# Performance work log

Hardware: AMD Instinct MI355X
Metric: run time of the kernel (lower is better)

The kernel has to match this reference:

```python
import jax, jax.numpy as jnp
import numpy as np

B, S, D = 4, 2048, 1024
H, DQ, DV = 16, 64, 64
LN_EPS = 1e-3  # keras LayerNormalization default


def _layer_norm(x, gamma, beta):
    mu = jnp.mean(x, axis=-1, keepdims=True)
    var = jnp.mean(jnp.square(x - mu), axis=-1, keepdims=True)
    return (x - mu) * jax.lax.rsqrt(var + LN_EPS) * gamma + beta


def setup_inputs() -> dict:
    key = jax.random.key(0)
    ks = jax.random.split(key, 6)
    x = jax.random.normal(ks[0], (B, S, D), jnp.float32)
    lengths = jax.random.randint(ks[1], (B,), 1, S + 1).astype(jnp.int32)
    scale = 0.02
    return {
        "query_sequences": x,
        "key_value_sequences": x,  # identical -> self-attention branch
        "key_value_sequence_lengths": lengths,
        "W_q": jax.random.normal(ks[2], (D, H * DQ), jnp.float32) * scale,
        "b_q": jnp.zeros((H * DQ,), jnp.float32),
        "W_kv": jax.random.normal(ks[3], (D, H * (DQ + DV)), jnp.float32) * scale,
        "b_kv": jnp.zeros((H * (DQ + DV),), jnp.float32),
        "W_o": jax.random.normal(ks[4], (H * DV, D), jnp.float32) * scale,
        "b_o": jnp.zeros((D,), jnp.float32),
        "ln_gamma": jnp.ones((D,), jnp.float32),
        "ln_beta": jnp.zeros((D,), jnp.float32),
    }


def reference(query_sequences, key_value_sequences, key_value_sequence_lengths,
              W_q, b_q, W_kv, b_kv, W_o, b_o, ln_gamma, ln_beta):
    # data-dependent self-attention detection, as in the TF code
    self_att = jnp.all(query_sequences == key_value_sequences)

    q_norm = _layer_norm(query_sequences, ln_gamma, ln_beta)
    kv_used = jnp.where(self_att, _layer_norm(key_value_sequences, ln_gamma, ln_beta),
                        key_value_sequences)
    residual = q_norm

    Q = (q_norm @ W_q + b_q).reshape(B, S, H, DQ)          # b q h d
    KV = kv_used @ W_kv + b_kv
    K = KV[..., : H * DQ].reshape(B, S, H, DQ)              # b k h d
    V = KV[..., H * DQ :].reshape(B, S, H, DV)              # b k h d

    scores = jnp.einsum("bqhd,bkhd->bhqk", Q, K) / np.sqrt(DQ).astype(np.float32)

    # key padding mask: key position < true length
    not_pad = (jnp.arange(S, dtype=jnp.int32)[None, None, None, :]
               < key_value_sequence_lengths[:, None, None, None])
    scores = jnp.where(not_pad, scores, -jnp.inf)
    # in_decoder=False -> no causal mask branch

    attn = jax.nn.softmax(scores, axis=-1)                  # dropout is identity at inference
    ctx = jnp.einsum("bhqk,bkhd->bqhd", attn, V).reshape(B, S, H * DV)
    out = ctx @ W_o + b_o + residual
    return out
```

## Files before the change

kernel.cpp:

```cpp
#include <hip/hip_runtime.h>
#include <hip/hip_bf16.h>
#include <cstdint>
#include <cmath>


#define DEV static __device__ __forceinline__

typedef float  f32x4 __attribute__((ext_vector_type(4)));
typedef short  s16x8 __attribute__((ext_vector_type(8)));
typedef short  s16x4 __attribute__((ext_vector_type(4)));
typedef __bf16 bf16x8 __attribute__((ext_vector_type(8)));
typedef unsigned int u32x4 __attribute__((ext_vector_type(4)));

DEV void gload_lds16(const void* g, void* l) {
  __builtin_amdgcn_global_load_lds(
      (const __attribute__((address_space(1))) unsigned int*)g,
      (__attribute__((address_space(3))) unsigned int*)l, 16, 0, 0);
}

DEV bf16x8 ldsv(const void* p) {
  return __builtin_bit_cast(bf16x8, *(const s16x8*)p);
}

DEV f32x4 mfma16(bf16x8 a, bf16x8 b, f32x4 c) {
  return __builtin_amdgcn_mfma_f32_16x16x32_bf16(a, b, c, 0, 0, 0);
}

DEV unsigned short f2b(float f) {
  __hip_bfloat16 h = __float2bfloat16(f);
  return __builtin_bit_cast(unsigned short, h);
}

DEV unsigned int cvt_pk_bf16(float lo, float hi) {
  unsigned int r;
  asm("v_cvt_pk_bf16_f32 %0, %1, %2" : "=v"(r) : "v"(lo), "v"(hi));
  return r;
}

__global__ __launch_bounds__(256) void ln_kernel(
    const float* __restrict__ x, const float* __restrict__ gamma,
    const float* __restrict__ beta, __hip_bfloat16* __restrict__ out)
{
  const int row = blockIdx.x, t = threadIdx.x;
  const float4 v = ((const float4*)(x + (size_t)row * 1024))[t];
  float s = v.x + v.y + v.z + v.w;
  float q = v.x * v.x + v.y * v.y + v.z * v.z + v.w * v.w;
#pragma unroll
  for (int m = 1; m < 64; m <<= 1) { s += __shfl_xor(s, m, 64); q += __shfl_xor(q, m, 64); }
  __shared__ float red[8];
  if ((t & 63) == 0) { red[t >> 6] = s; red[4 + (t >> 6)] = q; }
  __syncthreads();
  s = red[0] + red[1] + red[2] + red[3];
  q = red[4] + red[5] + red[6] + red[7];
  const float mu = s * (1.f / 1024.f);
  const float var = q * (1.f / 1024.f) - mu * mu;
  const float rs = rsqrtf(var + 1e-3f);
  const float4 g = ((const float4*)gamma)[t];
  const float4 bt = ((const float4*)beta)[t];
  s16x4 o;
  o[0] = (short)f2b((v.x - mu) * rs * g.x + bt.x);
  o[1] = (short)f2b((v.y - mu) * rs * g.y + bt.y);
  o[2] = (short)f2b((v.z - mu) * rs * g.z + bt.z);
  o[3] = (short)f2b((v.w - mu) * rs * g.w + bt.w);
  *(s16x4*)((short*)out + (size_t)row * 1024 + t * 4) = o;
}

__global__ __launch_bounds__(256) void wconv(
    const float* __restrict__ W, int N, __hip_bfloat16* __restrict__ Wt)
{
  __shared__ float tile[64][65];
  const int t = threadIdx.x;
  const int k0 = blockIdx.x * 64, n0 = blockIdx.y * 64;
#pragma unroll
  for (int p = 0; p < 4; ++p) {
    int r = p * 16 + (t >> 4), c4 = (t & 15) * 4;
    float4 v = *(const float4*)(W + (size_t)(k0 + r) * N + n0 + c4);
    tile[r][c4] = v.x; tile[r][c4 + 1] = v.y; tile[r][c4 + 2] = v.z; tile[r][c4 + 3] = v.w;
  }
  __syncthreads();
#pragma unroll
  for (int p = 0; p < 4; ++p) {
    int n = p * 16 + (t >> 4), kc = (t & 15) * 4;
    s16x4 o;
    o[0] = (short)f2b(tile[kc][n]);     o[1] = (short)f2b(tile[kc + 1][n]);
    o[2] = (short)f2b(tile[kc + 2][n]); o[3] = (short)f2b(tile[kc + 3][n]);
    *(s16x4*)((short*)Wt + (size_t)(n0 + n) * 1024 + k0 + kc) = o;
  }
}

template<bool RESID>
__global__ __launch_bounds__(256, 2) void gemm_bt(
    const __hip_bfloat16* __restrict__ A, const __hip_bfloat16* __restrict__ Bt,
    const float* __restrict__ bias0, const float* __restrict__ bias1, int split,
    const __hip_bfloat16* __restrict__ resid,
    __hip_bfloat16* __restrict__ outb, float* __restrict__ outf, int Ncols)
{
  __shared__ __align__(16) short sA[128 * 64];
  __shared__ __align__(16) short sB[128 * 64];
  const int t = threadIdx.x, l = t & 63, w = t >> 6;
  const int wr = w >> 1, wc = w & 1, lr = l & 15, lg = l >> 4;
  const int row0 = blockIdx.y * 128, col0 = blockIdx.x * 128;
  f32x4 acc[4][4] = {};

  for (int kt = 0; kt < 1024; kt += 64) {
#pragma unroll
    for (int p = 0; p < 4; ++p) {
      const int L = p * 4096 + t * 16;
      const int r = L >> 7, c = ((L >> 4) & 7) ^ (r & 7);
      gload_lds16((const char*)A + ((size_t)(row0 + r) * 1024 + kt + c * 8) * 2, (char*)sA + L);
    }
#pragma unroll
    for (int p = 0; p < 4; ++p) {
      const int L = p * 4096 + t * 16;
      const int r = L >> 7, c = ((L >> 4) & 7) ^ (r & 7);
      gload_lds16((const char*)Bt + ((size_t)(col0 + r) * 1024 + kt + c * 8) * 2, (char*)sB + L);
    }
    __syncthreads();

    bf16x8 af[4][2], bfr[4][2];
#pragma unroll
    for (int mb = 0; mb < 4; ++mb) {
      const int ar = wr * 64 + mb * 16 + lr;
#pragma unroll
      for (int kk = 0; kk < 2; ++kk)
        af[mb][kk] = ldsv((const char*)sA + ar * 128 + (((kk * 4 + lg) ^ (ar & 7)) * 16));
    }
#pragma unroll
    for (int nb = 0; nb < 4; ++nb) {
      const int br = wc * 64 + nb * 16 + lr;
#pragma unroll
      for (int kk = 0; kk < 2; ++kk)
        bfr[nb][kk] = ldsv((const char*)sB + br * 128 + (((kk * 4 + lg) ^ (br & 7)) * 16));
    }
#pragma unroll
    for (int kk = 0; kk < 2; ++kk)
#pragma unroll
      for (int mb = 0; mb < 4; ++mb)
#pragma unroll
        for (int nb = 0; nb < 4; ++nb)
          acc[mb][nb] = mfma16(af[mb][kk], bfr[nb][kk], acc[mb][nb]);
    __syncthreads();
  }

#pragma unroll
  for (int mb = 0; mb < 4; ++mb) {
    const int rbase = row0 + wr * 64 + mb * 16 + lg * 4;
#pragma unroll
    for (int nb = 0; nb < 4; ++nb) {
      const int col = col0 + wc * 64 + nb * 16 + lr;
      const float bias = (col < split) ? bias0[col] : bias1[col - split];
#pragma unroll
      for (int jr = 0; jr < 4; ++jr) {
        const size_t idx = (size_t)(rbase + jr) * Ncols + col;
        float v = acc[mb][nb][jr] + bias;
        if (RESID) outf[idx] = v + __bfloat162float(resid[idx]);
        else       outb[idx] = __float2bfloat16(v);
      }
    }
  }
}

__global__ __launch_bounds__(256) void vtrans(
    const __hip_bfloat16* __restrict__ qkv, __hip_bfloat16* __restrict__ vt)
{
  __shared__ __align__(16) short tile[64][72];
  const int t = threadIdx.x;
  const int s0 = blockIdx.x * 64;
  const int bh = blockIdx.y, b = bh >> 4, h = bh & 15;
#pragma unroll
  for (int p = 0; p < 2; ++p) {
    int idx = p * 256 + t;
    int r = idx >> 3, c = idx & 7;
    s16x8 vv = *(const s16x8*)((const short*)qkv +
        (size_t)(b * 2048 + s0 + r) * 3072 + 2048 + h * 64 + c * 8);
    *(s16x8*)((char*)tile + r * 144 + c * 16) = vv;
  }
  __syncthreads();
  const int dv = t >> 2, sc = (t & 3) * 16;
  s16x8 a, bvec;
#pragma unroll
  for (int e = 0; e < 8; ++e) a[e] = tile[sc + e][dv];
#pragma unroll
  for (int e = 0; e < 8; ++e) bvec[e] = tile[sc + 8 + e][dv];
  short* dst = (short*)vt + (size_t)(bh * 64 + dv) * 2048 + s0 + sc;
  *(s16x8*)dst = a;
  *(s16x8*)(dst + 8) = bvec;
}

__global__ __launch_bounds__(256, 4) void attn_kernel(
    const __hip_bfloat16* __restrict__ qkv, const __hip_bfloat16* __restrict__ vt,
    const int* __restrict__ lens, __hip_bfloat16* __restrict__ ctx)
{
  __shared__ __align__(16) short sK[2][64 * 64];
  __shared__ __align__(16) short sV[2][64 * 64];
  const int t = threadIdx.x, l = t & 63, w = t >> 6;
  const int lr = l & 15, lg = l >> 4;
  const int bh = blockIdx.y, b = bh >> 4, h = bh & 15;
  const int q0 = blockIdx.x * 128 + w * 32;
  const int len = lens[b];
  const float NEG = -__builtin_inff();
  const float QSC = 0.18033688f;

  bf16x8 qf[2][2];
#pragma unroll
  for (int mbt = 0; mbt < 2; ++mbt)
#pragma unroll
    for (int kk = 0; kk < 2; ++kk) {
      bf16x8 r = ldsv((const char*)qkv +
          ((size_t)(b * 2048 + q0 + mbt * 16 + lr) * 3072 + h * 64 + kk * 32 + lg * 8) * 2);
#pragma unroll
      for (int e = 0; e < 8; ++e) qf[mbt][kk][e] = (__bf16)((float)r[e] * QSC);
    }

  f32x4 o[4][2] = {};
  float mrun[2] = {NEG, NEG}, ssum[2] = {0.f, 0.f};

  auto stage = [&](short* dK, short* dV, int kv0) {
#pragma unroll
    for (int p = 0; p < 2; ++p) {
      const int L = p * 4096 + t * 16;
      const int r = L >> 7, c = ((L >> 4) & 7) ^ (r & 7);
      gload_lds16((const char*)qkv +
          ((size_t)(b * 2048 + kv0 + r) * 3072 + 1024 + h * 64 + c * 8) * 2, (char*)dK + L);
    }
#pragma unroll
    for (int p = 0; p < 2; ++p) {
      const int L = p * 4096 + t * 16;
      const int r = L >> 7, c = ((L >> 4) & 7) ^ (r & 7);
      gload_lds16((const char*)vt +
          ((size_t)(bh * 64 + r) * 2048 + kv0 + c * 8) * 2, (char*)dV + L);
    }
  };

  const int nt = (len + 63) >> 6;
  short* curK = sK[0]; short* nxtK = sK[1];
  short* curV = sV[0]; short* nxtV = sV[1];
  stage(curK, curV, 0);

  const int srcA = (lg & 1) * 32 + lr;
  const int srcB = srcA + 16;

  for (int ti = 0; ti < nt; ++ti) {
    const int kv0 = ti * 64;
    if (ti + 1 < nt) {
      stage(nxtK, nxtV, kv0 + 64);
      asm volatile("s_waitcnt vmcnt(4)" ::: "memory");
    } else {
      asm volatile("s_waitcnt vmcnt(0)" ::: "memory");
    }
    __builtin_amdgcn_s_barrier();
    asm volatile("" ::: "memory");

    f32x4 sf[2][4] = {};
    __builtin_amdgcn_s_setprio(1);
#pragma unroll
    for (int kk = 0; kk < 2; ++kk) {
      bf16x8 ak[4];
#pragma unroll
      for (int nbt = 0; nbt < 4; ++nbt) {
        const int br = nbt * 16 + lr;
        ak[nbt] = ldsv((const char*)curK + br * 128 + (((kk * 4 + lg) ^ (br & 7)) * 16));
      }
#pragma unroll
      for (int mbt = 0; mbt < 2; ++mbt)
#pragma unroll
        for (int nbt = 0; nbt < 4; ++nbt)
          sf[mbt][nbt] = mfma16(ak[nbt], qf[mbt][kk], sf[mbt][nbt]);
    }
    __builtin_amdgcn_s_setprio(0);

    if (kv0 + 64 > len) {
#pragma unroll
      for (int nbt = 0; nbt < 4; ++nbt)
#pragma unroll
        for (int jr = 0; jr < 4; ++jr)
          if (kv0 + nbt * 16 + lg * 4 + jr >= len) {
            sf[0][nbt][jr] = NEG;
            sf[1][nbt][jr] = NEG;
          }
    }

    float rm[2];
#pragma unroll
    for (int mbt = 0; mbt < 2; ++mbt) {
      f32x4 m4 = sf[mbt][0];
      m4 = __builtin_elementwise_max(m4, sf[mbt][1]);
      m4 = __builtin_elementwise_max(m4, sf[mbt][2]);
      m4 = __builtin_elementwise_max(m4, sf[mbt][3]);
      float m0 = fmaxf(fmaxf(m4[0], m4[1]), fmaxf(m4[2], m4[3]));
      m0 = fmaxf(m0, __shfl_xor(m0, 16, 64));
      m0 = fmaxf(m0, __shfl_xor(m0, 32, 64));
      rm[mbt] = m0;
    }
    const bool need = (rm[0] > mrun[0] + 3.f) || (rm[1] > mrun[1] + 3.f);
    if (__any(need)) {
#pragma unroll
      for (int mbt = 0; mbt < 2; ++mbt) {
        const float mnew = fmaxf(mrun[mbt], rm[mbt]);
        const float corr = __builtin_amdgcn_exp2f(mrun[mbt] - mnew);
        mrun[mbt] = mnew;
        ssum[mbt] *= corr;
#pragma unroll
        for (int nbt2 = 0; nbt2 < 4; ++nbt2) o[nbt2][mbt] *= corr;
      }
    }
    unsigned int W0[2][4], W1[2][4];
#pragma unroll
    for (int mbt = 0; mbt < 2; ++mbt) {
      f32x4 ts = {0.f, 0.f, 0.f, 0.f};
#pragma unroll
      for (int nbt = 0; nbt < 4; ++nbt) {
        f32x4 pe;
#pragma unroll
        for (int jr = 0; jr < 4; ++jr)
          pe[jr] = __builtin_amdgcn_exp2f(sf[mbt][nbt][jr] - mrun[mbt]);
        ts += pe;
        W0[mbt][nbt] = cvt_pk_bf16(pe[0], pe[1]);
        W1[mbt][nbt] = cvt_pk_bf16(pe[2], pe[3]);
      }
      ssum[mbt] += (ts[0] + ts[1]) + (ts[2] + ts[3]);
    }

#pragma unroll
    for (int c = 0; c < 2; ++c) {
      bf16x8 vf[4], pb[2];
#pragma unroll
      for (int nbt2 = 0; nbt2 < 4; ++nbt2) {
        const int vr = nbt2 * 16 + lr;
        vf[nbt2] = ldsv((const char*)curV + vr * 128 + (((c * 4 + lg) ^ (vr & 7)) * 16));
      }
#pragma unroll
      for (int mbt = 0; mbt < 2; ++mbt) {
        const unsigned int selW0 = (lg & 2) ? W0[mbt][2 * c + 1] : W0[mbt][2 * c];
        const unsigned int selW1 = (lg & 2) ? W1[mbt][2 * c + 1] : W1[mbt][2 * c];
        u32x4 bw;
        bw[0] = __shfl((int)selW0, srcA, 64);
        bw[1] = __shfl((int)selW1, srcA, 64);
        bw[2] = __shfl((int)selW0, srcB, 64);
        bw[3] = __shfl((int)selW1, srcB, 64);
        pb[mbt] = __builtin_bit_cast(bf16x8, bw);
      }
      __builtin_amdgcn_s_setprio(1);
#pragma unroll
      for (int nbt2 = 0; nbt2 < 4; ++nbt2)
#pragma unroll
        for (int mbt = 0; mbt < 2; ++mbt)
          o[nbt2][mbt] = mfma16(vf[nbt2], pb[mbt], o[nbt2][mbt]);
      __builtin_amdgcn_s_setprio(0);
    }

    asm volatile("s_waitcnt lgkmcnt(0)" ::: "memory");
    __builtin_amdgcn_s_barrier();
    asm volatile("" ::: "memory");
    short* tk = curK; curK = nxtK; nxtK = tk;
    short* tv = curV; curV = nxtV; nxtV = tv;
  }

  float inv[2];
#pragma unroll
  for (int mbt = 0; mbt < 2; ++mbt) {
    float s = ssum[mbt];
    s += __shfl_xor(s, 16, 64);
    s += __shfl_xor(s, 32, 64);
    inv[mbt] = 1.f / s;
  }
  char* eb = (char*)sK + w * 4352;
#pragma unroll
  for (int mbt = 0; mbt < 2; ++mbt)
#pragma unroll
    for (int nbt2 = 0; nbt2 < 4; ++nbt2)
#pragma unroll
      for (int jr = 0; jr < 4; ++jr)
        *(short*)(eb + (mbt * 16 + lr) * 136 + (nbt2 * 16 + lg * 4 + jr) * 2) =
            (short)f2b(o[nbt2][mbt][jr] * inv[mbt]);
  asm volatile("s_waitcnt lgkmcnt(0)" ::: "memory");
  __builtin_amdgcn_sched_barrier(0);
  const int qi = l >> 1, half = l & 1;
#pragma unroll
  for (int i = 0; i < 4; ++i) {
    s16x8 v = *(const s16x8*)(eb + qi * 136 + half * 64 + i * 16);
    *(s16x8*)((short*)ctx + (size_t)(b * 2048 + q0 + qi) * 1024 + h * 64 + half * 32 + i * 8) = v;
  }
}

extern "C" void kernel_launch(void* const* d_in, const int* in_sizes, int n_in,
                              void* d_out, int out_size, void* d_ws, size_t ws_size,
                              hipStream_t stream)
{
  const float* x     = (const float*)d_in[0];
  const int*   lens  = (const int*)d_in[2];
  const float* Wq    = (const float*)d_in[3];
  const float* bq    = (const float*)d_in[4];
  const float* Wkv   = (const float*)d_in[5];
  const float* bkv   = (const float*)d_in[6];
  const float* Wo    = (const float*)d_in[7];
  const float* bo    = (const float*)d_in[8];
  const float* gamma = (const float*)d_in[9];
  const float* beta  = (const float*)d_in[10];
  float* out = (float*)d_out;

  char* ws = (char*)d_ws;
  __hip_bfloat16* ln  = (__hip_bfloat16*)(ws);
  __hip_bfloat16* qkv = (__hip_bfloat16*)(ws + ((size_t)16 << 20));
  __hip_bfloat16* vt  = (__hip_bfloat16*)(ws + ((size_t)64 << 20));
  __hip_bfloat16* ctx = (__hip_bfloat16*)(ws + ((size_t)80 << 20));
  __hip_bfloat16* wt  = (__hip_bfloat16*)(ws + ((size_t)96 << 20));
  __hip_bfloat16* wot = (__hip_bfloat16*)(ws + ((size_t)102 << 20));

  ln_kernel<<<dim3(8192), dim3(256), 0, stream>>>(x, gamma, beta, ln);
  wconv<<<dim3(16, 16), dim3(256), 0, stream>>>(Wq, 1024, wt);
  wconv<<<dim3(16, 32), dim3(256), 0, stream>>>(Wkv, 2048, wt + (size_t)1024 * 1024);
  wconv<<<dim3(16, 16), dim3(256), 0, stream>>>(Wo, 1024, wot);
  gemm_bt<false><<<dim3(24, 64), dim3(256), 0, stream>>>(
      ln, wt, bq, bkv, 1024, (const __hip_bfloat16*)nullptr,
      qkv, (float*)nullptr, 3072);
  vtrans<<<dim3(32, 64), dim3(256), 0, stream>>>(qkv, vt);
  attn_kernel<<<dim3(16, 64), dim3(256), 0, stream>>>(qkv, vt, lens, ctx);
  gemm_bt<true><<<dim3(8, 64), dim3(256), 0, stream>>>(
      ctx, wot, bo, bo, 1 << 30, ln,
      (__hip_bfloat16*)nullptr, out, 1024);
}
```

Baseline: 174.9 us.

## Replace QKV projection GEMM with 256x256-tile, triple-buffered 8-wave kernel

Adds a new QKV projection kernel using 512 threads, 256x256 output tiles and K-steps of 32 with three LDS buffers. It interleaves A and B staging between two half-MFMA phases separated by barriers, and remaps block IDs across XCD-like groups for cache locality. The goal is more operand reuse per tile and better overlap of global loads with MFMA work. It also specialises the output-projection GEMM by removing the template. The cost is more barriers per iteration and higher register and LDS pressure (96KB LDS per block).

```diff
diff --git a/kernel.cpp b/kernel.cpp
--- a/kernel.cpp
+++ b/kernel.cpp
@@ -36,6 +36,8 @@
   asm("v_cvt_pk_bf16_f32 %0, %1, %2" : "=v"(r) : "v"(lo), "v"(hi));
   return r;
 }
+
+#define MEMFENCE asm volatile("" ::: "memory")
 
 __global__ __launch_bounds__(256) void ln_kernel(
     const float* __restrict__ x, const float* __restrict__ gamma,
@@ -88,12 +90,113 @@
   }
 }
 
-template<bool RESID>
+__global__ __launch_bounds__(512, 2) void gemm8(
+    const __hip_bfloat16* __restrict__ A, const __hip_bfloat16* __restrict__ Bt,
+    const float* __restrict__ bias0, const float* __restrict__ bias1, int split,
+    __hip_bfloat16* __restrict__ outb)
+{
+  __shared__ __align__(16) short sA[3 * 8192];
+  __shared__ __align__(16) short sB[3 * 8192];
+  const int t = threadIdx.x, l = t & 63, w = t >> 6;
+  const int wr = w >> 2, wc = w & 3, lr = l & 15, lg = l >> 4;
+  int bid = blockIdx.x;
+  const int cpx = gridDim.x >> 3;
+  bid = (bid & 7) * cpx + (bid >> 3);
+  const int bx = bid % 12, by = bid / 12;
+  const int row0 = by * 256, col0 = bx * 256;
+
+  f32x4 acc[8][4] = {};
+  const int NT = 32;
+
+  auto stageA = [&](int buf, int kt) {
+#pragma unroll
+    for (int p = 0; p < 2; ++p) {
+      const int L = p * 8192 + t * 16;
+      const int r = L >> 6, c = (L >> 4) & 3;
+      const int j = c ^ (r & 3);
+      gload_lds16((const char*)A + ((size_t)(row0 + r) * 1024 + kt + j * 8) * 2,
+                  (char*)sA + buf * 16384 + L);
+    }
+  };
+  auto stageB = [&](int buf, int kt) {
+#pragma unroll
+    for (int p = 0; p < 2; ++p) {
+      const int L = p * 8192 + t * 16;
+      const int r = L >> 6, c = (L >> 4) & 3;
+      const int j = c ^ (r & 3);
+      gload_lds16((const char*)Bt + ((size_t)(col0 + r) * 1024 + kt + j * 8) * 2,
+                  (char*)sB + buf * 16384 + L);
+    }
+  };
+
+  stageA(0, 0);  stageB(0, 0);
+  stageA(1, 32); stageB(1, 32);
+  asm volatile("s_waitcnt vmcnt(4)" ::: "memory");
+  MEMFENCE; __builtin_amdgcn_s_barrier(); MEMFENCE;
+
+#pragma unroll 1
+  for (int ti = 0; ti < NT; ++ti) {
+    const int cur = ti % 3, nx2 = (ti + 2) % 3;
+    const char* bA = (const char*)sA + cur * 16384;
+    const char* bB = (const char*)sB + cur * 16384;
+    bf16x8 bfr[4], af[4];
+#pragma unroll
+    for (int nb = 0; nb < 4; ++nb) {
+      const int br = wc * 64 + nb * 16 + lr;
+      bfr[nb] = ldsv(bB + br * 64 + ((lg ^ (br & 3)) * 16));
+    }
+#pragma unroll
+    for (int mb = 0; mb < 4; ++mb) {
+      const int ar = wr * 128 + mb * 16 + lr;
+      af[mb] = ldsv(bA + ar * 64 + ((lg ^ (ar & 3)) * 16));
+    }
+    if (ti + 2 < NT) stageA(nx2, (ti + 2) * 32);
+    MEMFENCE; __builtin_amdgcn_s_barrier(); MEMFENCE;
+    __builtin_amdgcn_s_setprio(1);
+#pragma unroll
+    for (int mb = 0; mb < 4; ++mb)
+#pragma unroll
+      for (int nb = 0; nb < 4; ++nb)
+        acc[mb][nb] = mfma16(af[mb], bfr[nb], acc[mb][nb]);
+    __builtin_amdgcn_s_setprio(0);
+    MEMFENCE; __builtin_amdgcn_s_barrier(); MEMFENCE;
+#pragma unroll
+    for (int mb = 0; mb < 4; ++mb) {
+      const int ar = wr * 128 + 64 + mb * 16 + lr;
+      af[mb] = ldsv(bA + ar * 64 + ((lg ^ (ar & 3)) * 16));
+    }
+    if (ti + 2 < NT) stageB(nx2, (ti + 2) * 32);
+    MEMFENCE; __builtin_amdgcn_s_barrier(); MEMFENCE;
+    __builtin_amdgcn_s_setprio(1);
+#pragma unroll
+    for (int mb = 0; mb < 4; ++mb)
+#pragma unroll
+      for (int nb = 0; nb < 4; ++nb)
+        acc[mb + 4][nb] = mfma16(af[mb], bfr[nb], acc[mb + 4][nb]);
+    __builtin_amdgcn_s_setprio(0);
+    if (ti + 2 < NT) asm volatile("s_waitcnt vmcnt(4)" ::: "memory");
+    else             asm volatile("s_waitcnt vmcnt(0)" ::: "memory");
+    MEMFENCE; __builtin_amdgcn_s_barrier(); MEMFENCE;
+  }
+
+#pragma unroll
+  for (int mb = 0; mb < 8; ++mb) {
+    const int rbase = row0 + wr * 128 + mb * 16 + lg * 4;
+#pragma unroll
+    for (int nb = 0; nb < 4; ++nb) {
+      const int col = col0 + wc * 64 + nb * 16 + lr;
+      const float bias = (col < split) ? bias0[col] : bias1[col - split];
+#pragma unroll
+      for (int jr = 0; jr < 4; ++jr)
+        outb[(size_t)(rbase + jr) * 3072 + col] = __float2bfloat16(acc[mb][nb][jr] + bias);
+    }
+  }
+}
+
 __global__ __launch_bounds__(256, 2) void gemm_bt(
     const __hip_bfloat16* __restrict__ A, const __hip_bfloat16* __restrict__ Bt,
-    const float* __restrict__ bias0, const float* __restrict__ bias1, int split,
-    const __hip_bfloat16* __restrict__ resid,
-    __hip_bfloat16* __restrict__ outb, float* __restrict__ outf, int Ncols)
+    const float* __restrict__ bias0,
+    const __hip_bfloat16* __restrict__ resid, float* __restrict__ outf)
 {
   __shared__ __align__(16) short sA[128 * 64];
   __shared__ __align__(16) short sB[128 * 64];
@@ -148,13 +251,11 @@
 #pragma unroll
     for (int nb = 0; nb < 4; ++nb) {
       const int col = col0 + wc * 64 + nb * 16 + lr;
-      const float bias = (col < split) ? bias0[col] : bias1[col - split];
+      const float bias = bias0[col];
 #pragma unroll
       for (int jr = 0; jr < 4; ++jr) {
-        const size_t idx = (size_t)(rbase + jr) * Ncols + col;
-        float v = acc[mb][nb][jr] + bias;
-        if (RESID) outf[idx] = v + __bfloat162float(resid[idx]);
-        else       outb[idx] = __float2bfloat16(v);
+        const size_t idx = (size_t)(rbase + jr) * 1024 + col;
+        outf[idx] = acc[mb][nb][jr] + bias + __bfloat162float(resid[idx]);
       }
     }
   }
@@ -248,8 +349,7 @@
     } else {
       asm volatile("s_waitcnt vmcnt(0)" ::: "memory");
     }
-    __builtin_amdgcn_s_barrier();
-    asm volatile("" ::: "memory");
+    MEMFENCE; __builtin_amdgcn_s_barrier(); MEMFENCE;
 
     f32x4 sf[2][4] = {};
     __builtin_amdgcn_s_setprio(1);
@@ -350,8 +450,7 @@
     }
 
     asm volatile("s_waitcnt lgkmcnt(0)" ::: "memory");
-    __builtin_amdgcn_s_barrier();
-    asm volatile("" ::: "memory");
+    MEMFENCE; __builtin_amdgcn_s_barrier(); MEMFENCE;
     short* tk = curK; curK = nxtK; nxtK = tk;
     short* tv = curV; curV = nxtV; nxtV = tv;
   }
@@ -411,12 +510,8 @@
   wconv<<<dim3(16, 16), dim3(256), 0, stream>>>(Wq, 1024, wt);
   wconv<<<dim3(16, 32), dim3(256), 0, stream>>>(Wkv, 2048, wt + (size_t)1024 * 1024);
   wconv<<<dim3(16, 16), dim3(256), 0, stream>>>(Wo, 1024, wot);
-  gemm_bt<false><<<dim3(24, 64), dim3(256), 0, stream>>>(
-      ln, wt, bq, bkv, 1024, (const __hip_bfloat16*)nullptr,
-      qkv, (float*)nullptr, 3072);
+  gemm8<<<dim3(384), dim3(512), 0, stream>>>(ln, wt, bq, bkv, 1024, qkv);
   vtrans<<<dim3(32, 64), dim3(256), 0, stream>>>(qkv, vt);
   attn_kernel<<<dim3(16, 64), dim3(256), 0, stream>>>(qkv, vt, lens, ctx);
-  gemm_bt<true><<<dim3(8, 64), dim3(256), 0, stream>>>(
-      ctx, wot, bo, bo, 1 << 30, ln,
-      (__hip_bfloat16*)nullptr, out, 1024);
-}
+  gemm_bt<<<dim3(8, 64), dim3(256), 0, stream>>>(ctx, wot, bo, ln, out);
+}
```

New measurement: 188.9 us. +8.0%, slower.
